# Kernel tuning notes

Hardware: AMD Instinct MI355X
Metric: run time of the kernel (lower is better)

## Reference

```python
import jax, jax.numpy as jnp
import numpy as np

N_NODE = 200000   # item catalog size (n_node)
EMB = 100         # emb_size
NNZ = 1000000     # hypergraph adjacency nonzeros
B = 1024          # batch / cl_size
L = 50            # session length
LAYERS = 2        # HyperConv layers (opt.layer)
TAU = 0.2         # contrastive temperature
K_NEI = 3         # FindNeighbors.neighbor_n


def setup_inputs() -> dict:
    key = jax.random.key(0)
    ks = jax.random.split(key, 16)
    g = 1.414 / np.sqrt(EMB)  # xavier_normal gain=1.414 scale
    inp = {}
    inp["embedding"] = jax.random.normal(ks[0], (N_NODE, EMB), jnp.float32) * 0.1
    inp["adj_val"] = jax.random.uniform(ks[1], (NNZ,), jnp.float32)
    inp["A"] = jax.random.uniform(ks[2], (B, B), jnp.float32) * 0.01
    inp["D"] = jax.random.uniform(ks[3], (B, B), jnp.float32) * 0.01
    inp["z2"] = jax.random.normal(ks[4], (B, EMB), jnp.float32)
    inp["Wcf1"] = jax.random.normal(ks[5], (EMB, EMB), jnp.float32) * g
    inp["bcf1"] = jnp.zeros((EMB,), jnp.float32)
    inp["Wcf2"] = jax.random.normal(ks[6], (EMB, EMB), jnp.float32) * g
    inp["bcf2"] = jnp.zeros((EMB,), jnp.float32)
    inp["Wkg1"] = jax.random.normal(ks[7], (EMB, EMB), jnp.float32) * g
    inp["bkg1"] = jnp.zeros((EMB,), jnp.float32)
    inp["Wkg2"] = jax.random.normal(ks[8], (EMB, EMB), jnp.float32) * g
    inp["bkg2"] = jnp.zeros((EMB,), jnp.float32)
    inp["session_len"] = jnp.full((B, 1), float(L), jnp.float32)
    inp["adj_row"] = jax.random.randint(ks[9], (NNZ,), 0, N_NODE, jnp.int32)
    inp["adj_col"] = jax.random.randint(ks[10], (NNZ,), 0, N_NODE, jnp.int32)
    inp["items"] = jax.random.randint(ks[11], (B, L), 0, N_NODE + 1, jnp.int32)
    return inp


def _proj(z, W1, b1, W2, b2):
    # nn.Linear -> ELU -> nn.Linear (Contrast_2view projector)
    return jax.nn.elu(z @ W1.T + b1) @ W2.T + b2


def reference(embedding, adj_val, A, D, z2,
              Wcf1, bcf1, Wcf2, bcf2, Wkg1, bkg1, Wkg2, bkg2,
              session_len, adj_row, adj_col, items):
    # ---- HyperConv: layered sparse propagation, averaged over layers ----
    h = embedding
    acc = embedding
    for _ in range(LAYERS):
        # torch.sparse.mm(adjacency, h) via gather + segment_sum
        h = jax.ops.segment_sum(adj_val[:, None] * h[adj_col], adj_row,
                                num_segments=N_NODE)
        acc = acc + h
    hyper = acc / (LAYERS + 1)  # [N_NODE, EMB]

    # ---- RelationGAT.forward ----
    emb_pad = jnp.concatenate([jnp.zeros((1, EMB), hyper.dtype), hyper], axis=0)
    seq_h = emb_pad[items]                       # [B, L, EMB]
    rel = jnp.sum(seq_h, axis=1) / session_len   # [B, EMB]
    rel = (D @ A) @ rel                          # session-graph conv
    c = jax.nn.selu(rel)
    l_c = c / jnp.linalg.norm(c, axis=-1, keepdims=True)  # [B, EMB]

    # ---- FindNeighbors (dropout omitted: eval mode) ----
    sess = l_c
    norms = jnp.sqrt(jnp.sum(sess * sess + 1e-6, axis=1, keepdims=True))
    cos = (sess @ sess.T) / (norms @ norms.T)    # [B, B]
    cos = jax.nn.softmax(cos, axis=-1)
    topv, topi = jax.lax.top_k(cos, K_NEI)       # [B, K]
    topv = jax.nn.softmax(topv, axis=-1)
    neighbor = jnp.sum(topv[:, :, None] * sess[topi], axis=1)  # [B, EMB]

    # ---- Contrast_2view ----
    z1p = _proj(sess, Wcf1, bcf1, Wcf2, bcf2)
    z2p = _proj(z2, Wkg1, bkg1, Wkg2, bkg2)
    n1 = jnp.linalg.norm(z1p, axis=-1, keepdims=True)
    n2 = jnp.linalg.norm(z2p, axis=-1, keepdims=True)
    simm = jnp.exp((z1p @ z2p.T) / (n1 @ n2.T) / TAU)
    simm = simm / (jnp.sum(simm, axis=1, keepdims=True) + 1e-8)
    cl_loss = -jnp.mean(jnp.log(jnp.diagonal(simm)))  # pos = eye

    return hyper, l_c, neighbor, cl_loss
```

## Files before the change

kernel.cpp:

```cpp
#include <hip/hip_runtime.h>
#include <hip/hip_bf16.h>

#define N_NODE 200000
#define EMB 100
#define NNZ 1000000
#define BATCH 1024
#define SLEN 50
#define BE (BATCH * EMB)
#define SCAN_BLK 1024
#define PROJ_ROWS 8

#define OFF_LC    20000000LL
#define OFF_NB    20102400LL
#define OFF_LOSS  20204800LL

typedef __hip_bfloat16 bf16;

__device__ __forceinline__ float b2f(bf16 x) { return __bfloat162float(x); }
__device__ __forceinline__ bf16 f2b(float x) { return __float2bfloat16(x); }

__device__ __forceinline__ float ldf(const void* p, long long i, int f32) {
    return f32 ? ((const float*)p)[i] : b2f(((const bf16*)p)[i]);
}
__device__ __forceinline__ void stf(void* p, long long i, int f32, float v) {
    if (f32) ((float*)p)[i] = v;
    else     ((bf16*)p)[i] = f2b(v);
}

__device__ __forceinline__ float bfb2f(unsigned short s) {
    return __uint_as_float(((unsigned)s) << 16);
}
__device__ __forceinline__ unsigned short f2bfb(float x) {
    bf16 h = f2b(x); unsigned short r; __builtin_memcpy(&r, &h, 2); return r;
}
__device__ __forceinline__ float2 up2(unsigned u) {
    return make_float2(bfb2f((unsigned short)(u & 0xffff)), bfb2f((unsigned short)(u >> 16)));
}
__device__ __forceinline__ unsigned pk2(float a, float b) {
    return (unsigned)f2bfb(a) | ((unsigned)f2bfb(b) << 16);
}
__device__ __forceinline__ float2 ldf2(const void* p, long long pi, int f32) {
    if (f32) return ((const float2*)p)[pi];
    return up2(((const unsigned*)p)[pi]);
}
__device__ __forceinline__ void stf2(void* p, long long pi, int f32, float a, float b) {
    if (f32) ((float2*)p)[pi] = make_float2(a, b);
    else     ((unsigned*)p)[pi] = pk2(a, b);
}

__device__ __forceinline__ float wave_allreduce_sum(float v) {
    for (int m = 32; m > 0; m >>= 1) v += __shfl_xor(v, m, 64);
    return v;
}

__global__ void hist_kernel(const int* __restrict__ rows, int* __restrict__ counts,
                            const void* __restrict__ adjval, int* __restrict__ flag) {
    if (blockIdx.x == 0 && threadIdx.x == 0) {
        int f = 0;
        const bf16* p = (const bf16*)adjval;
        for (int i = 0; i < 64; i++) {
            float x = b2f(p[i]);
            if (!(x >= 0.0f && x <= 1.0f)) f = 1;
        }
        *flag = f;
    }
    int e = blockIdx.x * 256 + threadIdx.x;
    if (e < NNZ) atomicAdd(&counts[rows[e]], 1);
}

__global__ void scan_block(const int* __restrict__ counts, int* __restrict__ incl,
                           int* __restrict__ bsums) {
    __shared__ int s[SCAN_BLK];
    int i = blockIdx.x * SCAN_BLK + threadIdx.x;
    int v = (i < N_NODE) ? counts[i] : 0;
    s[threadIdx.x] = v;
    __syncthreads();
    for (int off = 1; off < SCAN_BLK; off <<= 1) {
        int add = (threadIdx.x >= (unsigned)off) ? s[threadIdx.x - off] : 0;
        __syncthreads();
        s[threadIdx.x] += add;
        __syncthreads();
    }
    if (i < N_NODE) incl[i] = s[threadIdx.x];
    if (threadIdx.x == SCAN_BLK - 1) bsums[blockIdx.x] = s[threadIdx.x];
}

__global__ void scan_top(int* __restrict__ bsums, int nb) {
    __shared__ int s[256];
    int t = threadIdx.x;
    int v = (t < nb) ? bsums[t] : 0;
    s[t] = v;
    __syncthreads();
    for (int off = 1; off < 256; off <<= 1) {
        int add = (t >= off) ? s[t - off] : 0;
        __syncthreads();
        s[t] += add;
        __syncthreads();
    }
    if (t < nb) bsums[t] = s[t] - v;
}

__global__ void scan_add(const int* __restrict__ counts, const int* __restrict__ incl,
                         const int* __restrict__ bsums, int* __restrict__ row_ptr,
                         int* __restrict__ cursor) {
    int i = blockIdx.x * SCAN_BLK + threadIdx.x;
    if (i < N_NODE) {
        int ex = incl[i] - counts[i] + bsums[blockIdx.x];
        row_ptr[i] = ex;
        cursor[i] = ex;
    }
    if (i == 0) row_ptr[N_NODE] = NNZ;
}

__global__ void permute_edges(const int* __restrict__ arow, const int* __restrict__ acol,
                              const void* __restrict__ aval, int* __restrict__ cursor,
                              int* __restrict__ colp, float* __restrict__ valp,
                              const int* __restrict__ flagp) {
    const int f32 = *flagp;
    int e = blockIdx.x * 256 + threadIdx.x;
    if (e >= NNZ) return;
    int r = arow[e];
    int pos = atomicAdd(&cursor[r], 1);
    colp[pos] = acol[e];
    valp[pos] = ldf(aval, e, f32);
}

__global__ __launch_bounds__(256) void spmm_gather1(
        const int* __restrict__ rp, const int* __restrict__ colp,
        const float* __restrict__ valp, const void* __restrict__ emb,
        unsigned* __restrict__ h1, const int* __restrict__ flagp) {
    const int f32 = *flagp;
    int lane = threadIdx.x & 63;
    int r = blockIdx.x * 4 + (threadIdx.x >> 6);
    if (r >= N_NODE || lane >= 50) return;
    int k0 = rp[r], k1 = rp[r + 1];
    float a0 = 0.f, a1 = 0.f;
    for (int k = k0; k < k1; k++) {
        int cl = colp[k];
        float v = valp[k];
        float2 e = ldf2(emb, (long long)cl * 50 + lane, f32);
        a0 += v * e.x; a1 += v * e.y;
    }
    h1[(long long)r * 50 + lane] = pk2(a0, a1);
}

__global__ __launch_bounds__(256) void spmm_gather2(
        const int* __restrict__ rp, const int* __restrict__ colp,
        const float* __restrict__ valp, const void* __restrict__ emb,
        const unsigned* __restrict__ h1, void* __restrict__ out,
        const int* __restrict__ flagp) {
    const int f32 = *flagp;
    int lane = threadIdx.x & 63;
    int r = blockIdx.x * 4 + (threadIdx.x >> 6);
    if (r >= N_NODE || lane >= 50) return;
    int k0 = rp[r], k1 = rp[r + 1];
    float a0 = 0.f, a1 = 0.f;
    for (int k = k0; k < k1; k++) {
        int cl = colp[k];
        float v = valp[k];
        float2 e = up2(h1[(long long)cl * 50 + lane]);
        a0 += v * e.x; a1 += v * e.y;
    }
    float2 eb = ldf2(emb, (long long)r * 50 + lane, f32);
    float2 h1r = up2(h1[(long long)r * 50 + lane]);
    stf2(out, (long long)r * 50 + lane, f32,
         (eb.x + h1r.x + a0) * (1.0f / 3.0f), (eb.y + h1r.y + a1) * (1.0f / 3.0f));
}

__global__ __launch_bounds__(256) void rel_rows(
        const void* __restrict__ out, const int* __restrict__ items,
        const void* __restrict__ slen, float* __restrict__ rel,
        const int* __restrict__ flagp) {
    const int f32 = *flagp;
    int lane = threadIdx.x & 63;
    int b = blockIdx.x * 4 + (threadIdx.x >> 6);
    if (b >= BATCH || lane >= 50) return;
    float s0 = 0.f, s1 = 0.f;
    for (int l = 0; l < SLEN; l++) {
        int it = items[b * SLEN + l];
        if (it > 0) {
            float2 e = ldf2(out, (long long)(it - 1) * 50 + lane, f32);
            s0 += e.x; s1 += e.y;
        }
    }
    float inv = 1.0f / ldf(slen, b, f32);
    ((float2*)rel)[b * 50 + lane] = make_float2(s0 * inv, s1 * inv);
}

__global__ __launch_bounds__(256) void bmm_rows(const void* __restrict__ M,
                                                const float* __restrict__ X,
                                                float* __restrict__ Y,
                                                const int* __restrict__ flagp) {
    __shared__ float ms[4][BATCH];
    const int f32 = *flagp;
    int i0 = blockIdx.x * 4;
    int t = threadIdx.x;
    for (int idx = t; idx < 4 * BATCH; idx += 256) {
        int rr = idx >> 10, j = idx & 1023;
        ms[rr][j] = ldf(M, (long long)(i0 + rr) * BATCH + j, f32);
    }
    __syncthreads();
    int w = t >> 6, lane = t & 63;
    if (lane >= 50) return;
    int i = i0 + w;
    const float2* X2 = (const float2*)X;
    float s0 = 0.f, s1 = 0.f;
    for (int j = 0; j < BATCH; j++) {
        float m = ms[w][j];
        float2 x = X2[j * 50 + lane];
        s0 += m * x.x; s1 += m * x.y;
    }
    ((float2*)Y)[i * 50 + lane] = make_float2(s0, s1);
}

__global__ void selu_norm(const float* __restrict__ rel2, float* __restrict__ sess,
                          float* __restrict__ sessT, float* __restrict__ ns,
                          void* __restrict__ out, const int* __restrict__ flagp) {
    const int f32 = *flagp;
    int b = blockIdx.x, t = threadIdx.x;
    const float sc = 1.0507009873554804934193349852946f;
    const float al = 1.6732632423543772848170429916717f;
    float x0 = (t < EMB) ? rel2[b * EMB + t] : 0.f;
    float x1 = (t + 64 < EMB) ? rel2[b * EMB + t + 64] : 0.f;
    float c0 = (x0 > 0.f) ? sc * x0 : sc * (al * expm1f(x0));
    float c1 = (x1 > 0.f) ? sc * x1 : sc * (al * expm1f(x1));
    if (t >= EMB) c0 = 0.f;
    if (t + 64 >= EMB) c1 = 0.f;
    float nrm = sqrtf(wave_allreduce_sum(c0 * c0 + c1 * c1));
    float l0 = c0 / nrm, l1 = c1 / nrm;
    float nterm = 0.f;
    if (t < EMB) {
        sess[b * EMB + t] = l0;
        sessT[t * BATCH + b] = l0;
        stf(out, OFF_LC + b * EMB + t, f32, l0);
        nterm += l0 * l0 + 1e-6f;
    }
    if (t + 64 < EMB) {
        sess[b * EMB + t + 64] = l1;
        sessT[(t + 64) * BATCH + b] = l1;
        stf(out, OFF_LC + b * EMB + t + 64, f32, l1);
        nterm += l1 * l1 + 1e-6f;
    }
    float n2sum = wave_allreduce_sum(nterm);
    if (t == 0) ns[b] = sqrtf(n2sum);
}

__global__ void neighbor_kernel(const float* __restrict__ sess, const float* __restrict__ sessT,
                                const float* __restrict__ ns, void* __restrict__ out,
                                const int* __restrict__ flagp) {
    __shared__ float si[EMB];
    __shared__ float red[4];
    __shared__ float wrv[4]; __shared__ int wri[4];
    __shared__ float chv[3]; __shared__ int chi[3];
    __shared__ float stv[3];
    const int f32 = *flagp;
    int i = blockIdx.x, t = threadIdx.x;
    if (t < EMB) si[t] = sess[i * EMB + t];
    __syncthreads();
    float ni = ns[i];
    float d0 = 0.f, d1 = 0.f, d2 = 0.f, d3 = 0.f;
    for (int k = 0; k < EMB; k++) {
        float sv = si[k];
        const float* row = sessT + k * BATCH;
        d0 += sv * row[t];
        d1 += sv * row[t + 256];
        d2 += sv * row[t + 512];
        d3 += sv * row[t + 768];
    }
    float pv0 = expf(d0 / (ni * ns[t]));
    float pv1 = expf(d1 / (ni * ns[t + 256]));
    float pv2 = expf(d2 / (ni * ns[t + 512]));
    float pv3 = expf(d3 / (ni * ns[t + 768]));
    float local = pv0 + pv1 + pv2 + pv3;
    float w = wave_allreduce_sum(local);
    if ((t & 63) == 0) red[t >> 6] = w;
    __syncthreads();
    float S = red[0] + red[1] + red[2] + red[3];

    int c0 = -1, c1 = -1, c2 = -1;
    float pv[4] = {pv0, pv1, pv2, pv3};
    for (int r = 0; r < 3; r++) {
        float bv = -1e30f; int bi = 0x7fffffff;
        #pragma unroll
        for (int m = 0; m < 4; m++) {
            int j = t + (m << 8);
            if (j == c0 || j == c1 || j == c2) continue;
            float v = pv[m];
            if (v > bv || (v == bv && j < bi)) { bv = v; bi = j; }
        }
        #pragma unroll
        for (int off = 1; off < 64; off <<= 1) {
            float ov = __shfl_xor(bv, off);
            int oi = __shfl_xor(bi, off);
            if (ov > bv || (ov == bv && oi < bi)) { bv = ov; bi = oi; }
        }
        if ((t & 63) == 0) { wrv[t >> 6] = bv; wri[t >> 6] = bi; }
        __syncthreads();
        if (t == 0) {
            float fv = wrv[0]; int fi = wri[0];
            for (int wq = 1; wq < 4; wq++) {
                if (wrv[wq] > fv || (wrv[wq] == fv && wri[wq] < fi)) { fv = wrv[wq]; fi = wri[wq]; }
            }
            chv[r] = fv; chi[r] = fi;
        }
        __syncthreads();
        if (r == 0) c0 = chi[0];
        else if (r == 1) c1 = chi[1];
        else c2 = chi[2];
    }
    if (t == 0) {
        float e0 = expf(chv[0] / S), e1 = expf(chv[1] / S), e2 = expf(chv[2] / S);
        float es = e0 + e1 + e2;
        stv[0] = e0 / es; stv[1] = e1 / es; stv[2] = e2 / es;
    }
    __syncthreads();
    if (t < EMB) {
        float o = stv[0] * sess[chi[0] * EMB + t]
                + stv[1] * sess[chi[1] * EMB + t]
                + stv[2] * sess[chi[2] * EMB + t];
        stf(out, OFF_NB + i * EMB + t, f32, o);
    }
}

__global__ __launch_bounds__(256) void proj2(
        const void* __restrict__ X, int x_dual,
        const void* __restrict__ W1, const void* __restrict__ B1,
        const void* __restrict__ W2, const void* __restrict__ B2,
        float* __restrict__ Z, float* __restrict__ ZT, float* __restrict__ nrm,
        const int* __restrict__ flagp) {
    __shared__ float wT[EMB * EMB];
    __shared__ float bsh[EMB];
    __shared__ float hid[PROJ_ROWS][EMB];
    __shared__ float xr[2][EMB];
    __shared__ float red2[2][2];
    const int f32 = *flagp;
    int t = threadIdx.x;
    int sub = t >> 7, u = t & 127;
    int r0 = blockIdx.x * PROJ_ROWS;
    for (int idx = t; idx < EMB * EMB; idx += 256) {
        int o = idx / EMB, k = idx - o * EMB;
        wT[k * EMB + o] = ldf(W1, idx, f32);
    }
    if (t < EMB) bsh[t] = ldf(B1, t, f32);
    __syncthreads();
    for (int pr = 0; pr < PROJ_ROWS; pr += 2) {
        int row = r0 + pr + sub;
        if (u < EMB)
            xr[sub][u] = x_dual ? ldf(X, (long long)row * EMB + u, f32)
                                : ((const float*)X)[row * EMB + u];
        __syncthreads();
        if (u < EMB) {
            float s = bsh[u];
            for (int k = 0; k < EMB; k++) s += xr[sub][k] * wT[k * EMB + u];
            hid[pr + sub][u] = (s > 0.f) ? s : expm1f(s);
        }
        __syncthreads();
    }
    for (int idx = t; idx < EMB * EMB; idx += 256) {
        int o = idx / EMB, k = idx - o * EMB;
        wT[k * EMB + o] = ldf(W2, idx, f32);
    }
    if (t < EMB) bsh[t] = ldf(B2, t, f32);
    __syncthreads();
    for (int pr = 0; pr < PROJ_ROWS; pr += 2) {
        int row = r0 + pr + sub;
        float sq = 0.f;
        if (u < EMB) {
            float o = bsh[u];
            const float* h = hid[pr + sub];
            for (int k = 0; k < EMB; k++) o += h[k] * wT[k * EMB + u];
            Z[(long long)row * EMB + u] = o;
            if (ZT) ZT[(long long)u * BATCH + row] = o;
            sq = o * o;
        }
        sq = wave_allreduce_sum(sq);
        int w = t >> 6;
        if ((t & 63) == 0) red2[sub][w & 1] = sq;
        __syncthreads();
        if (u == 0) nrm[row] = sqrtf(red2[sub][0] + red2[sub][1]);
        __syncthreads();
    }
}

__global__ void loss_kernel(const float* __restrict__ z1p, const float* __restrict__ z2pT,
                            const float* __restrict__ n1, const float* __restrict__ n2,
                            float* __restrict__ acc) {
    __shared__ float zi[EMB];
    __shared__ float red[4];
    __shared__ float sdiag;
    int i = blockIdx.x, t = threadIdx.x;
    if (t < EMB) zi[t] = z1p[i * EMB + t];
    __syncthreads();
    float ni = n1[i];
    float d0 = 0.f, d1 = 0.f, d2 = 0.f, d3 = 0.f;
    for (int k = 0; k < EMB; k++) {
        float zv = zi[k];
        const float* row = z2pT + k * BATCH;
        d0 += zv * row[t];
        d1 += zv * row[t + 256];
        d2 += zv * row[t + 512];
        d3 += zv * row[t + 768];
    }
    float e0 = expf(d0 / (ni * n2[t]) * 5.0f);
    float e1 = expf(d1 / (ni * n2[t + 256]) * 5.0f);
    float e2 = expf(d2 / (ni * n2[t + 512]) * 5.0f);
    float e3 = expf(d3 / (ni * n2[t + 768]) * 5.0f);
    if (t == (i & 255)) {
        int m = i >> 8;
        sdiag = (m == 0) ? e0 : (m == 1) ? e1 : (m == 2) ? e2 : e3;
    }
    float local = e0 + e1 + e2 + e3;
    float w = wave_allreduce_sum(local);
    if ((t & 63) == 0) red[t >> 6] = w;
    __syncthreads();
    if (t == 0) {
        float S = red[0] + red[1] + red[2] + red[3];
        float l = -logf(sdiag / (S + 1e-8f));
        atomicAdd(acc, l * (1.0f / BATCH));
    }
}

__global__ void write_loss(const float* __restrict__ acc, void* __restrict__ out,
                           const int* __restrict__ flagp) {
    stf(out, OFF_LOSS, *flagp, acc[0]);
}

extern "C" void kernel_launch(void* const* d_in, const int* in_sizes, int n_in,
                              void* d_out, int out_size, void* d_ws, size_t ws_size,
                              hipStream_t stream) {
    const void* emb  = d_in[0];
    const void* aval = d_in[1];
    const void* Amat = d_in[2];
    const void* Dmat = d_in[3];
    const void* z2   = d_in[4];
    const void* Wcf1 = d_in[5];
    const void* bcf1 = d_in[6];
    const void* Wcf2 = d_in[7];
    const void* bcf2 = d_in[8];
    const void* Wkg1 = d_in[9];
    const void* bkg1 = d_in[10];
    const void* Wkg2 = d_in[11];
    const void* bkg2 = d_in[12];
    const void* slen = d_in[13];
    const int* arow  = (const int*)d_in[14];
    const int* acol  = (const int*)d_in[15];
    const int* items = (const int*)d_in[16];

    int* flag      = (int*)d_ws;
    int* counts    = (int*)((char*)d_ws + 256);
    int* cursor    = counts;
    int* row_ptr   = counts + N_NODE;
    int* bsums     = row_ptr + N_NODE + 64;
    int* colp      = bsums + 256;
    float* valp    = (float*)(colp + NNZ);
    unsigned* h1buf = (unsigned*)(valp + NNZ);
    float* fsmall  = (float*)(h1buf + (long long)N_NODE * 50);
    float* rel   = fsmall;
    float* t1    = rel  + BE;
    float* rel2  = t1   + BE;
    float* sess  = rel2 + BE;
    float* sessT = sess + BE;
    float* z1p   = sessT + BE;
    float* z2p   = z1p  + BE;
    float* z2pT  = z2p  + BE;
    float* ns    = z2pT + BE;
    float* n1    = ns + BATCH;
    float* n2    = n1 + BATCH;
    float* lacc  = n2 + BATCH;

    const int nscan = (N_NODE + SCAN_BLK - 1) / SCAN_BLK;

    hipMemsetAsync(counts, 0, (size_t)N_NODE * sizeof(int), stream);
    hist_kernel<<<(NNZ + 255) / 256, 256, 0, stream>>>(arow, counts, aval, flag);
    scan_block<<<nscan, SCAN_BLK, 0, stream>>>(counts, colp, bsums);
    scan_top<<<1, 256, 0, stream>>>(bsums, nscan);
    scan_add<<<nscan, SCAN_BLK, 0, stream>>>(counts, colp, bsums, row_ptr, cursor);
    permute_edges<<<(NNZ + 255) / 256, 256, 0, stream>>>(arow, acol, aval, cursor,
                                                         colp, valp, flag);

    spmm_gather1<<<(N_NODE + 3) / 4, 256, 0, stream>>>(row_ptr, colp, valp, emb, h1buf, flag);
    spmm_gather2<<<(N_NODE + 3) / 4, 256, 0, stream>>>(row_ptr, colp, valp, emb, h1buf,
                                                       d_out, flag);

    rel_rows<<<(BATCH + 3) / 4, 256, 0, stream>>>(d_out, items, slen, rel, flag);
    bmm_rows<<<BATCH / 4, 256, 0, stream>>>(Amat, rel, t1, flag);
    bmm_rows<<<BATCH / 4, 256, 0, stream>>>(Dmat, t1, rel2, flag);
    selu_norm<<<BATCH, 64, 0, stream>>>(rel2, sess, sessT, ns, d_out, flag);

    neighbor_kernel<<<BATCH, 256, 0, stream>>>(sess, sessT, ns, d_out, flag);

    proj2<<<BATCH / PROJ_ROWS, 256, 0, stream>>>(sess, 0, Wcf1, bcf1, Wcf2, bcf2,
                                                 z1p, nullptr, n1, flag);
    proj2<<<BATCH / PROJ_ROWS, 256, 0, stream>>>(z2, 1, Wkg1, bkg1, Wkg2, bkg2,
                                                 z2p, z2pT, n2, flag);
    hipMemsetAsync(lacc, 0, sizeof(float), stream);
    loss_kernel<<<BATCH, 256, 0, stream>>>(z1p, z2pT, n1, n2, lacc);
    write_loss<<<1, 1, 0, stream>>>(lacc, d_out, flag);
}
```

Baseline: 789.7 us.

## Pack CSR col/val into int2 and unroll SpMM gathers for memory-level parallelism

Edge column indices and values are interleaved into a single int2 array, so each SpMM step reads one 8-byte entry instead of two separate arrays. Both SpMM gather kernels and the session-row gather now unroll by 8 (and 10), issuing several independent embedding loads before accumulating, which hides gather latency. The dtype flag is hoisted into template specialisation so the inner loops carry no per-element branch. Out-of-range tail slots are clamped and masked with zero weight, which costs redundant loads on short rows and raises register use.

```diff
diff --git a/kernel.cpp b/kernel.cpp
--- a/kernel.cpp
+++ b/kernel.cpp
@@ -9,6 +9,7 @@
 #define BE (BATCH * EMB)
 #define SCAN_BLK 1024
 #define PROJ_ROWS 8
+#define UNR 8
 
 #define OFF_LC    20000000LL
 #define OFF_NB    20102400LL
@@ -41,6 +42,11 @@
 }
 __device__ __forceinline__ float2 ldf2(const void* p, long long pi, int f32) {
     if (f32) return ((const float2*)p)[pi];
+    return up2(((const unsigned*)p)[pi]);
+}
+template<bool F32>
+__device__ __forceinline__ float2 ldf2t(const void* p, long long pi) {
+    if (F32) return ((const float2*)p)[pi];
     return up2(((const unsigned*)p)[pi]);
 }
 __device__ __forceinline__ void stf2(void* p, long long pi, int f32, float a, float b) {
@@ -114,77 +120,130 @@
 
 __global__ void permute_edges(const int* __restrict__ arow, const int* __restrict__ acol,
                               const void* __restrict__ aval, int* __restrict__ cursor,
-                              int* __restrict__ colp, float* __restrict__ valp,
-                              const int* __restrict__ flagp) {
+                              int2* __restrict__ cv, const int* __restrict__ flagp) {
     const int f32 = *flagp;
     int e = blockIdx.x * 256 + threadIdx.x;
     if (e >= NNZ) return;
     int r = arow[e];
     int pos = atomicAdd(&cursor[r], 1);
-    colp[pos] = acol[e];
-    valp[pos] = ldf(aval, e, f32);
-}
-
-__global__ __launch_bounds__(256) void spmm_gather1(
-        const int* __restrict__ rp, const int* __restrict__ colp,
-        const float* __restrict__ valp, const void* __restrict__ emb,
-        unsigned* __restrict__ h1, const int* __restrict__ flagp) {
-    const int f32 = *flagp;
+    float v = ldf(aval, e, f32);
+    cv[pos] = make_int2(acol[e], __float_as_int(v));
+}
+
+template<bool F32>
+__device__ __forceinline__ void spmm1_body(
+        const int* __restrict__ rp, const int2* __restrict__ cv,
+        const void* __restrict__ emb, unsigned* __restrict__ h1) {
     int lane = threadIdx.x & 63;
     int r = blockIdx.x * 4 + (threadIdx.x >> 6);
     if (r >= N_NODE || lane >= 50) return;
     int k0 = rp[r], k1 = rp[r + 1];
     float a0 = 0.f, a1 = 0.f;
-    for (int k = k0; k < k1; k++) {
-        int cl = colp[k];
-        float v = valp[k];
-        float2 e = ldf2(emb, (long long)cl * 50 + lane, f32);
-        a0 += v * e.x; a1 += v * e.y;
+    for (int k = k0; k < k1; k += UNR) {
+        int2 c[UNR];
+        #pragma unroll
+        for (int j = 0; j < UNR; j++) {
+            int kk = k + j;
+            c[j] = cv[kk < k1 ? kk : k1 - 1];
+        }
+        float2 e[UNR];
+        #pragma unroll
+        for (int j = 0; j < UNR; j++)
+            e[j] = ldf2t<F32>(emb, (long long)c[j].x * 50 + lane);
+        #pragma unroll
+        for (int j = 0; j < UNR; j++) {
+            float v = (k + j < k1) ? __int_as_float(c[j].y) : 0.f;
+            a0 += v * e[j].x; a1 += v * e[j].y;
+        }
     }
     h1[(long long)r * 50 + lane] = pk2(a0, a1);
 }
 
-__global__ __launch_bounds__(256) void spmm_gather2(
-        const int* __restrict__ rp, const int* __restrict__ colp,
-        const float* __restrict__ valp, const void* __restrict__ emb,
-        const unsigned* __restrict__ h1, void* __restrict__ out,
-        const int* __restrict__ flagp) {
-    const int f32 = *flagp;
+__global__ __launch_bounds__(256) void spmm_gather1(
+        const int* __restrict__ rp, const int2* __restrict__ cv,
+        const void* __restrict__ emb,
+        unsigned* __restrict__ h1, const int* __restrict__ flagp) {
+    if (*flagp) spmm1_body<true>(rp, cv, emb, h1);
+    else        spmm1_body<false>(rp, cv, emb, h1);
+}
+
+template<bool F32>
+__device__ __forceinline__ void spmm2_body(
+        const int* __restrict__ rp, const int2* __restrict__ cv,
+        const void* __restrict__ emb,
+        const unsigned* __restrict__ h1, void* __restrict__ out) {
     int lane = threadIdx.x & 63;
     int r = blockIdx.x * 4 + (threadIdx.x >> 6);
     if (r >= N_NODE || lane >= 50) return;
     int k0 = rp[r], k1 = rp[r + 1];
     float a0 = 0.f, a1 = 0.f;
-    for (int k = k0; k < k1; k++) {
-        int cl = colp[k];
-        float v = valp[k];
-        float2 e = up2(h1[(long long)cl * 50 + lane]);
-        a0 += v * e.x; a1 += v * e.y;
-    }
-    float2 eb = ldf2(emb, (long long)r * 50 + lane, f32);
+    for (int k = k0; k < k1; k += UNR) {
+        int2 c[UNR];
+        #pragma unroll
+        for (int j = 0; j < UNR; j++) {
+            int kk = k + j;
+            c[j] = cv[kk < k1 ? kk : k1 - 1];
+        }
+        float2 e[UNR];
+        #pragma unroll
+        for (int j = 0; j < UNR; j++)
+            e[j] = up2(h1[(long long)c[j].x * 50 + lane]);
+        #pragma unroll
+        for (int j = 0; j < UNR; j++) {
+            float v = (k + j < k1) ? __int_as_float(c[j].y) : 0.f;
+            a0 += v * e[j].x; a1 += v * e[j].y;
+        }
+    }
+    float2 eb = ldf2t<F32>(emb, (long long)r * 50 + lane);
     float2 h1r = up2(h1[(long long)r * 50 + lane]);
-    stf2(out, (long long)r * 50 + lane, f32,
+    stf2(out, (long long)r * 50 + lane, F32 ? 1 : 0,
          (eb.x + h1r.x + a0) * (1.0f / 3.0f), (eb.y + h1r.y + a1) * (1.0f / 3.0f));
+}
+
+__global__ __launch_bounds__(256) void spmm_gather2(
+        const int* __restrict__ rp, const int2* __restrict__ cv,
+        const void* __restrict__ emb,
+        const unsigned* __restrict__ h1, void* __restrict__ out,
+        const int* __restrict__ flagp) {
+    if (*flagp) spmm2_body<true>(rp, cv, emb, h1, out);
+    else        spmm2_body<false>(rp, cv, emb, h1, out);
+}
+
+template<bool F32>
+__device__ __forceinline__ void rel_rows_body(
+        const void* __restrict__ out, const int* __restrict__ items,
+        const void* __restrict__ slen, float* __restrict__ rel) {
+    int lane = threadIdx.x & 63;
+    int b = blockIdx.x * 4 + (threadIdx.x >> 6);
+    if (b >= BATCH || lane >= 50) return;
+    float s0 = 0.f, s1 = 0.f;
+    #pragma unroll
+    for (int l0 = 0; l0 < SLEN; l0 += 10) {
+        int it[10];
+        #pragma unroll
+        for (int j = 0; j < 10; j++) it[j] = items[b * SLEN + l0 + j];
+        float2 e[10];
+        #pragma unroll
+        for (int j = 0; j < 10; j++) {
+            int idx = (it[j] > 0) ? it[j] - 1 : 0;
+            e[j] = ldf2t<F32>(out, (long long)idx * 50 + lane);
+        }
+        #pragma unroll
+        for (int j = 0; j < 10; j++) {
+            float m = (it[j] > 0) ? 1.f : 0.f;
+            s0 += m * e[j].x; s1 += m * e[j].y;
+        }
+    }
+    float inv = 1.0f / ldf(slen, b, F32 ? 1 : 0);
+    ((float2*)rel)[b * 50 + lane] = make_float2(s0 * inv, s1 * inv);
 }
 
 __global__ __launch_bounds__(256) void rel_rows(
         const void* __restrict__ out, const int* __restrict__ items,
         const void* __restrict__ slen, float* __restrict__ rel,
         const int* __restrict__ flagp) {
-    const int f32 = *flagp;
-    int lane = threadIdx.x & 63;
-    int b = blockIdx.x * 4 + (threadIdx.x >> 6);
-    if (b >= BATCH || lane >= 50) return;
-    float s0 = 0.f, s1 = 0.f;
-    for (int l = 0; l < SLEN; l++) {
-        int it = items[b * SLEN + l];
-        if (it > 0) {
-            float2 e = ldf2(out, (long long)(it - 1) * 50 + lane, f32);
-            s0 += e.x; s1 += e.y;
-        }
-    }
-    float inv = 1.0f / ldf(slen, b, f32);
-    ((float2*)rel)[b * 50 + lane] = make_float2(s0 * inv, s1 * inv);
+    if (*flagp) rel_rows_body<true>(out, items, slen, rel);
+    else        rel_rows_body<false>(out, items, slen, rel);
 }
 
 __global__ __launch_bounds__(256) void bmm_rows(const void* __restrict__ M,
@@ -451,9 +510,9 @@
     int* cursor    = counts;
     int* row_ptr   = counts + N_NODE;
     int* bsums     = row_ptr + N_NODE + 64;
-    int* colp      = bsums + 256;
-    float* valp    = (float*)(colp + NNZ);
-    unsigned* h1buf = (unsigned*)(valp + NNZ);
+    int2* cv       = (int2*)(bsums + 256);
+    int* scanbuf   = (int*)cv;
+    unsigned* h1buf = (unsigned*)(cv + NNZ);
     float* fsmall  = (float*)(h1buf + (long long)N_NODE * 50);
     float* rel   = fsmall;
     float* t1    = rel  + BE;
@@ -472,14 +531,14 @@
 
     hipMemsetAsync(counts, 0, (size_t)N_NODE * sizeof(int), stream);
     hist_kernel<<<(NNZ + 255) / 256, 256, 0, stream>>>(arow, counts, aval, flag);
-    scan_block<<<nscan, SCAN_BLK, 0, stream>>>(counts, colp, bsums);
+    scan_block<<<nscan, SCAN_BLK, 0, stream>>>(counts, scanbuf, bsums);
     scan_top<<<1, 256, 0, stream>>>(bsums, nscan);
-    scan_add<<<nscan, SCAN_BLK, 0, stream>>>(counts, colp, bsums, row_ptr, cursor);
+    scan_add<<<nscan, SCAN_BLK, 0, stream>>>(counts, scanbuf, bsums, row_ptr, cursor);
     permute_edges<<<(NNZ + 255) / 256, 256, 0, stream>>>(arow, acol, aval, cursor,
-                                                         colp, valp, flag);
-
-    spmm_gather1<<<(N_NODE + 3) / 4, 256, 0, stream>>>(row_ptr, colp, valp, emb, h1buf, flag);
-    spmm_gather2<<<(N_NODE + 3) / 4, 256, 0, stream>>>(row_ptr, colp, valp, emb, h1buf,
+                                                         cv, flag);
+
+    spmm_gather1<<<(N_NODE + 3) / 4, 256, 0, stream>>>(row_ptr, cv, emb, h1buf, flag);
+    spmm_gather2<<<(N_NODE + 3) / 4, 256, 0, stream>>>(row_ptr, cv, emb, h1buf,
                                                        d_out, flag);
 
     rel_rows<<<(BATCH + 3) / 4, 256, 0, stream>>>(d_out, items, slen, rel, flag);
```

Result: faster. 713.1 us (-9.7%).
